# Performance work log

Measured on AMD Instinct MI355X. Metric: run time of the kernel, lower is better.

## Reference

```python
import jax, jax.numpy as jnp
import numpy as np
import math

HEAD = 8
D_MODEL = 512
D_K = D_MODEL // HEAD
BS = 1024
HIST = 199


def setup_inputs() -> dict:
    key = jax.random.key(0)
    ks = jax.random.split(key, 9)
    s = 1.0 / math.sqrt(D_MODEL)
    return {
        "current_embed": jax.random.normal(ks[0], (BS, D_MODEL), dtype=jnp.float32),
        "previous_embed": jax.random.normal(ks[1], (BS, HIST, D_MODEL), dtype=jnp.float32),
        "local_attn_mask": jax.random.normal(ks[2], (BS, HIST + 1), dtype=jnp.float32),
        "Wq": jax.random.normal(ks[3], (D_MODEL, D_MODEL), dtype=jnp.float32) * s,
        "bq": jax.random.normal(ks[4], (D_MODEL,), dtype=jnp.float32) * s,
        "Wk": jax.random.normal(ks[5], (D_MODEL, D_MODEL), dtype=jnp.float32) * s,
        "bk": jax.random.normal(ks[6], (D_MODEL,), dtype=jnp.float32) * s,
        "Wv": jax.random.normal(ks[7], (D_MODEL, D_MODEL), dtype=jnp.float32) * s,
        "bv": jax.random.normal(ks[8], (D_MODEL,), dtype=jnp.float32) * s,
    }


def reference(current_embed, previous_embed, local_attn_mask, Wq, bq, Wk, bk, Wv, bv):
    bs = current_embed.shape[0]
    # all_time_embed: [bs, T, d] where T = hist + 1
    all_time = jnp.concatenate([previous_embed, current_embed[:, None, :]], axis=1)
    T = all_time.shape[1]
    # Q: single query per batch -> [bs, head, d_k]
    q = (current_embed @ Wq.T + bq).reshape(bs, HEAD, D_K)
    # K, V over full history -> [bs, T, head, d_k]
    k = (all_time @ Wk.T + bk).reshape(bs, T, HEAD, D_K)
    v = (all_time @ Wv.T + bv).reshape(bs, T, HEAD, D_K)
    # scores: [bs, head, T], scaled; additive mask broadcast over heads
    scores = jnp.einsum("bhd,bthd->bht", q, k) / math.sqrt(D_K)
    norm = jax.nn.softmax(scores + local_attn_mask[:, None, :], axis=-1)
    # weighted sum over time -> [bs, head, d_k] -> [bs, d_model]
    out = jnp.einsum("bht,bthd->bhd", norm, v)
    return out.reshape(bs, D_MODEL)
```

## Files before the change

kernel.cpp:

```cpp
#include <hip/hip_runtime.h>
#include <math.h>

#define DM 512
#define NH 8
#define BS 1024
#define HIST 199
#define TT 200

__device__ __forceinline__ float dot8(const float4& a0, const float4& a1,
                                      const float4& b0, const float4& b1) {
  float p = a0.x * b0.x;
  p = fmaf(a0.y, b0.y, p);
  p = fmaf(a0.z, b0.z, p);
  p = fmaf(a0.w, b0.w, p);
  p = fmaf(a1.x, b1.x, p);
  p = fmaf(a1.y, b1.y, p);
  p = fmaf(a1.z, b1.z, p);
  p = fmaf(a1.w, b1.w, p);
  return p;
}

__device__ __forceinline__ float wred64(float p) {
  p += __shfl_xor(p, 1);
  p += __shfl_xor(p, 2);
  p += __shfl_xor(p, 4);
  p += __shfl_xor(p, 8);
  p += __shfl_xor(p, 16);
  p += __shfl_xor(p, 32);
  return p;
}

__global__ __launch_bounds__(256, 4) void qproj_kernel(
    const float* __restrict__ cur, const float* __restrict__ Wq,
    const float* __restrict__ bq, float* __restrict__ q) {
  const int lane = threadIdx.x & 63;
  const int wave = threadIdx.x >> 6;
  const int bg = blockIdx.x >> 2;
  const int jq = blockIdx.x & 3;
  const int j0 = jq * 128 + wave * 32;
  float4 ca[4], cb[4];
#pragma unroll
  for (int bb = 0; bb < 4; ++bb) {
    const float* cp = cur + (size_t)(bg * 4 + bb) * DM;
    ca[bb] = *(const float4*)(cp + 4 * lane);
    cb[bb] = *(const float4*)(cp + 256 + 4 * lane);
  }
  float keep[2] = {0.f, 0.f};
  for (int r = 0; r < 32; ++r) {
    const float* wp = Wq + (size_t)(j0 + r) * DM;
    const float4 wa = *(const float4*)(wp + 4 * lane);
    const float4 wb = *(const float4*)(wp + 256 + 4 * lane);
    float pp[4];
#pragma unroll
    for (int bb = 0; bb < 4; ++bb)
      pp[bb] = wred64(dot8(ca[bb], cb[bb], wa, wb));
#pragma unroll
    for (int bb = 0; bb < 4; ++bb)
      if (lane == ((bb & 1) * 32 + r)) keep[bb >> 1] = pp[bb];
  }
  const int r = lane & 31, bh = lane >> 5;
  const int j = j0 + r;
#pragma unroll
  for (int s = 0; s < 2; ++s) {
    const int b = bg * 4 + 2 * s + bh;
    q[(size_t)b * DM + j] = keep[s] + bq[j];
  }
}

__global__ __launch_bounds__(256, 4) void qk_kernel(
    const float* __restrict__ q, const float* __restrict__ Wk,
    const float* __restrict__ bk, float* __restrict__ qk1,
    float* __restrict__ qc1) {
  __shared__ float q8[8][64];
  const int tid = threadIdx.x;
  const int bg = blockIdx.x >> 3;
  const int h = blockIdx.x & 7;
  for (int i = tid; i < 512; i += 256) {
    const int bl = i >> 6, d = i & 63;
    q8[bl][d] = q[(size_t)(bg * 8 + bl) * DM + h * 64 + d];
  }
  __syncthreads();
  float acc0[8], acc1[8];
#pragma unroll
  for (int bl = 0; bl < 8; ++bl) {
    acc0[bl] = 0.f;
    acc1[bl] = 0.f;
  }
  const int e = tid;
  const float* wkb = Wk + (size_t)h * 64 * DM;
  for (int d4 = 0; d4 < 64; d4 += 4) {
    float w0[4], w1[4];
#pragma unroll
    for (int dd = 0; dd < 4; ++dd) {
      w0[dd] = wkb[(size_t)(d4 + dd) * DM + e];
      w1[dd] = wkb[(size_t)(d4 + dd) * DM + e + 256];
    }
#pragma unroll
    for (int bl = 0; bl < 8; ++bl) {
      const float4 qq = *(const float4*)&q8[bl][d4];
      acc0[bl] = fmaf(qq.x, w0[0], acc0[bl]);
      acc0[bl] = fmaf(qq.y, w0[1], acc0[bl]);
      acc0[bl] = fmaf(qq.z, w0[2], acc0[bl]);
      acc0[bl] = fmaf(qq.w, w0[3], acc0[bl]);
      acc1[bl] = fmaf(qq.x, w1[0], acc1[bl]);
      acc1[bl] = fmaf(qq.y, w1[1], acc1[bl]);
      acc1[bl] = fmaf(qq.z, w1[2], acc1[bl]);
      acc1[bl] = fmaf(qq.w, w1[3], acc1[bl]);
    }
  }
#pragma unroll
  for (int bl = 0; bl < 8; ++bl) {
    const size_t base = ((size_t)(bg * 8 + bl) * NH + h) * DM;
    qk1[base + e] = acc0[bl] * 0.125f;
    qk1[base + e + 256] = acc1[bl] * 0.125f;
  }
  if (tid < 8) {
    float s = 0.f;
    for (int d = 0; d < 64; ++d) s += q8[tid][d] * bk[h * 64 + d];
    qc1[(size_t)(bg * 8 + tid) * NH + h] = s * 0.125f;
  }
}

__global__ __launch_bounds__(512, 4) void attn_kernel(
    const float* __restrict__ cur, const float* __restrict__ prev,
    const float* __restrict__ mask, const float* __restrict__ qk1,
    const float* __restrict__ qc1, const float* __restrict__ Wv,
    const float* __restrict__ bv, float* __restrict__ out) {
  __shared__ float red[2][4][DM];
  __shared__ float lred[2][4][4];
  const int tid = threadIdx.x;
  const int lane = tid & 63;
  const int wave = tid >> 6;
  const int g = wave & 1;
  const int c = wave >> 1;
  const int b = blockIdx.x;

  float4 ka[4], kb[4];
  float qc[4];
#pragma unroll
  for (int hl = 0; hl < 4; ++hl) {
    const float* kp = qk1 + ((size_t)b * NH + (g * 4 + hl)) * DM;
    ka[hl] = *(const float4*)(kp + 4 * lane);
    kb[hl] = *(const float4*)(kp + 256 + 4 * lane);
    qc[hl] = qc1[(size_t)b * NH + (g * 4 + hl)];
  }
  float4 cA[4], cB[4];
#pragma unroll
  for (int hl = 0; hl < 4; ++hl) {
    cA[hl] = make_float4(0.f, 0.f, 0.f, 0.f);
    cB[hl] = make_float4(0.f, 0.f, 0.f, 0.f);
  }
  float ls0 = 0.f, ls1 = 0.f, ls2 = 0.f, ls3 = 0.f;
  const int t0 = c * 50;
  const int nrows = (c == 3) ? 49 : 50;
  const int ml = (lane < 49) ? lane : 49;
  const float mreg = mask[(size_t)b * TT + t0 + ml];

#define ATTN_ROW(RA, RB, MIDX)                                         \
  {                                                                    \
    float pp[4];                                                       \
    _Pragma("unroll") for (int hl = 0; hl < 4; ++hl) pp[hl] =          \
        dot8(RA, RB, ka[hl], kb[hl]);                                  \
    _Pragma("unroll") for (int hl = 0; hl < 4; ++hl) pp[hl] =          \
        wred64(pp[hl]);                                                \
    const float mval = __shfl(mreg, (MIDX));                           \
    _Pragma("unroll") for (int hl = 0; hl < 4; ++hl) {                 \
      const float w = __expf(pp[hl] + qc[hl] + mval);                  \
      if (hl == 0) ls0 += w;                                           \
      if (hl == 1) ls1 += w;                                           \
      if (hl == 2) ls2 += w;                                           \
      if (hl == 3) ls3 += w;                                           \
      cA[hl].x = fmaf(w, RA.x, cA[hl].x);                              \
      cA[hl].y = fmaf(w, RA.y, cA[hl].y);                              \
      cA[hl].z = fmaf(w, RA.z, cA[hl].z);                              \
      cA[hl].w = fmaf(w, RA.w, cA[hl].w);                              \
      cB[hl].x = fmaf(w, RB.x, cB[hl].x);                              \
      cB[hl].y = fmaf(w, RB.y, cB[hl].y);                              \
      cB[hl].z = fmaf(w, RB.z, cB[hl].z);                              \
      cB[hl].w = fmaf(w, RB.w, cB[hl].w);                              \
    }                                                                  \
  }

  const float* pa = prev + ((size_t)b * HIST + t0) * DM + 4 * lane;
  float4 r0a = *(const float4*)(pa);
  float4 r0b = *(const float4*)(pa + 256);
  float4 r1a = *(const float4*)(pa + DM);
  float4 r1b = *(const float4*)(pa + DM + 256);
  for (int i = 0; i < nrows; ++i) {
    int ip = i + 2;
    if (ip >= nrows) ip = nrows - 1;
    const float* np = pa + (size_t)ip * DM;
    const float4 q0a = *(const float4*)(np);
    const float4 q0b = *(const float4*)(np + 256);
    ATTN_ROW(r0a, r0b, i)
    r0a = r1a;
    r0b = r1b;
    r1a = q0a;
    r1b = q0b;
  }
  if (c == 3) {
    const float* cp = cur + (size_t)b * DM + 4 * lane;
    const float4 xa = *(const float4*)(cp);
    const float4 xb = *(const float4*)(cp + 256);
    ATTN_ROW(xa, xb, 49)
  }
#undef ATTN_ROW

  if (lane == 0) {
    lred[g][c][0] = ls0;
    lred[g][c][1] = ls1;
    lred[g][c][2] = ls2;
    lred[g][c][3] = ls3;
  }
  for (int cc = 0; cc < 4; ++cc) {
    if (c == cc) {
#pragma unroll
      for (int hl = 0; hl < 4; ++hl) {
        float* dst = &red[g][hl][0];
        if (cc == 0) {
          *(float4*)(dst + 4 * lane) = cA[hl];
          *(float4*)(dst + 256 + 4 * lane) = cB[hl];
        } else {
          float4 o0 = *(const float4*)(dst + 4 * lane);
          float4 o1 = *(const float4*)(dst + 256 + 4 * lane);
          o0.x += cA[hl].x;
          o0.y += cA[hl].y;
          o0.z += cA[hl].z;
          o0.w += cA[hl].w;
          o1.x += cB[hl].x;
          o1.y += cB[hl].y;
          o1.z += cB[hl].z;
          o1.w += cB[hl].w;
          *(float4*)(dst + 4 * lane) = o0;
          *(float4*)(dst + 256 + 4 * lane) = o1;
        }
      }
    }
    __syncthreads();
  }
  const int hh = wave;
  const int g2 = hh >> 2, h2 = hh & 3;
  const float linv = 1.0f / (lred[g2][0][h2] + lred[g2][1][h2] +
                             lred[g2][2][h2] + lred[g2][3][h2]);
  const float4 na = *(const float4*)(&red[g2][h2][0] + 4 * lane);
  const float4 nb = *(const float4*)(&red[g2][h2][0] + 256 + 4 * lane);
  float keep = 0.f;
  for (int r = 0; r < 64; ++r) {
    const float* wvp = Wv + (size_t)(hh * 64 + r) * DM;
    const float4 wa = *(const float4*)(wvp + 4 * lane);
    const float4 wb = *(const float4*)(wvp + 256 + 4 * lane);
    float p = wred64(dot8(na, nb, wa, wb));
    if (lane == r) keep = p;
  }
  out[(size_t)b * DM + hh * 64 + lane] = keep * linv + bv[hh * 64 + lane];
}

extern "C" void kernel_launch(void* const* d_in, const int* in_sizes, int n_in,
                              void* d_out, int out_size, void* d_ws,
                              size_t ws_size, hipStream_t stream) {
  const float* cur = (const float*)d_in[0];
  const float* prev = (const float*)d_in[1];
  const float* mask = (const float*)d_in[2];
  const float* Wq = (const float*)d_in[3];
  const float* bq = (const float*)d_in[4];
  const float* Wk = (const float*)d_in[5];
  const float* bk = (const float*)d_in[6];
  const float* Wv = (const float*)d_in[7];
  const float* bv = (const float*)d_in[8];
  float* out = (float*)d_out;

  float* q = (float*)d_ws;
  float* qk1 = q + (size_t)BS * DM;
  float* qc1 = qk1 + (size_t)BS * NH * DM;

  qproj_kernel<<<1024, 256, 0, stream>>>(cur, Wq, bq, q);
  qk_kernel<<<1024, 256, 0, stream>>>(q, Wk, bk, qk1, qc1);
  attn_kernel<<<1024, 512, 0, stream>>>(cur, prev, mask, qk1, qc1, Wv, bv, out);
}
```

Before: 681.0 us.

## Split V projection into separate kernel batching 8 rows per Wv load

The per-head Wv projection moves out of the attention kernel's tail into a new kernel. The attention kernel now writes its normalized context vectors to workspace. Each block of the new kernel handles 8 batch rows for one head and reuses every Wv row load across those 8 rows, which cuts redundant Wv reads and shortens the attention kernel's serial tail. The cost is an extra launch and a round trip of a 16MB intermediate through global memory.

New measurement: 683.2 us. About the same (+0.3%).

```diff
diff --git a/kernel.cpp b/kernel.cpp
--- a/kernel.cpp
+++ b/kernel.cpp
@@ -124,8 +124,7 @@
 __global__ __launch_bounds__(512, 4) void attn_kernel(
     const float* __restrict__ cur, const float* __restrict__ prev,
     const float* __restrict__ mask, const float* __restrict__ qk1,
-    const float* __restrict__ qc1, const float* __restrict__ Wv,
-    const float* __restrict__ bv, float* __restrict__ out) {
+    const float* __restrict__ qc1, float* __restrict__ cn) {
   __shared__ float red[2][4][DM];
   __shared__ float lred[2][4][4];
   const int tid = threadIdx.x;
@@ -244,15 +243,46 @@
                              lred[g2][2][h2] + lred[g2][3][h2]);
   const float4 na = *(const float4*)(&red[g2][h2][0] + 4 * lane);
   const float4 nb = *(const float4*)(&red[g2][h2][0] + 256 + 4 * lane);
-  float keep = 0.f;
-  for (int r = 0; r < 64; ++r) {
-    const float* wvp = Wv + (size_t)(hh * 64 + r) * DM;
+  float* cp = cn + ((size_t)b * NH + hh) * DM;
+  *(float4*)(cp + 4 * lane) =
+      make_float4(na.x * linv, na.y * linv, na.z * linv, na.w * linv);
+  *(float4*)(cp + 256 + 4 * lane) =
+      make_float4(nb.x * linv, nb.y * linv, nb.z * linv, nb.w * linv);
+}
+
+__global__ __launch_bounds__(256, 4) void vproj_kernel(
+    const float* __restrict__ cn, const float* __restrict__ Wv,
+    const float* __restrict__ bv, float* __restrict__ out) {
+  const int lane = threadIdx.x & 63;
+  const int wave = threadIdx.x >> 6;
+  const int h = blockIdx.x & 7;
+  const int bg = blockIdx.x >> 3;
+  float4 na[8], nb[8];
+#pragma unroll
+  for (int bb = 0; bb < 8; ++bb) {
+    const float* cp = cn + ((size_t)(bg * 8 + bb) * NH + h) * DM;
+    na[bb] = *(const float4*)(cp + 4 * lane);
+    nb[bb] = *(const float4*)(cp + 256 + 4 * lane);
+  }
+  float keep[2] = {0.f, 0.f};
+  const int r0 = wave * 16;
+  for (int r = 0; r < 16; ++r) {
+    const float* wvp = Wv + (size_t)(h * 64 + r0 + r) * DM;
     const float4 wa = *(const float4*)(wvp + 4 * lane);
     const float4 wb = *(const float4*)(wvp + 256 + 4 * lane);
-    float p = wred64(dot8(na, nb, wa, wb));
-    if (lane == r) keep = p;
-  }
-  out[(size_t)b * DM + hh * 64 + lane] = keep * linv + bv[hh * 64 + lane];
+#pragma unroll
+    for (int bb = 0; bb < 8; ++bb) {
+      float p = wred64(dot8(na[bb], nb[bb], wa, wb));
+      if (lane == (bb * 8 + (r & 7))) keep[r >> 3] = p;
+    }
+  }
+  const int ob = lane >> 3, orr = lane & 7;
+  const int b = bg * 8 + ob;
+#pragma unroll
+  for (int s = 0; s < 2; ++s) {
+    const int j = h * 64 + r0 + s * 8 + orr;
+    out[(size_t)b * DM + j] = keep[s] + bv[j];
+  }
 }
 
 extern "C" void kernel_launch(void* const* d_in, const int* in_sizes, int n_in,
@@ -272,8 +302,10 @@
   float* q = (float*)d_ws;
   float* qk1 = q + (size_t)BS * DM;
   float* qc1 = qk1 + (size_t)BS * NH * DM;
+  float* cn = qc1 + (size_t)BS * NH;
 
   qproj_kernel<<<1024, 256, 0, stream>>>(cur, Wq, bq, q);
   qk_kernel<<<1024, 256, 0, stream>>>(q, Wk, bk, qk1, qc1);
-  attn_kernel<<<1024, 512, 0, stream>>>(cur, prev, mask, qk1, qc1, Wv, bv, out);
-}
+  attn_kernel<<<1024, 512, 0, stream>>>(cur, prev, mask, qk1, qc1, cn);
+  vproj_kernel<<<1024, 256, 0, stream>>>(cn, Wv, bv, out);
+}
```
